# Performance work log

Hardware: AMD Instinct MI355X
Metric: run time of the kernel (lower is better)

## Reference

```python
import jax, jax.numpy as jnp
import numpy as np

B, TGT, SRC, DIM = 8, 1024, 1024, 1024

def setup_inputs() -> dict:
    key = jax.random.key(0)
    k1, k2, k3, k4, k5 = jax.random.split(key, 5)
    s = 1.0 / np.sqrt(DIM)
    return {
        "input": jax.random.normal(k1, (B, TGT, DIM), dtype=jnp.float32),
        "context": jax.random.normal(k2, (B, SRC, DIM), dtype=jnp.float32),
        "context_lengths": jax.random.randint(k3, (B,), 1, SRC + 1, dtype=jnp.int64 if jax.config.jax_enable_x64 else jnp.int32),
        "W_in": jax.random.normal(k4, (DIM, DIM), dtype=jnp.float32) * s,   # torch Linear weight [out,in]
        "W_out": jax.random.normal(k5, (DIM, 2 * DIM), dtype=jnp.float32) * s,
    }

def reference(input, context, context_lengths, W_in, W_out):
    # GlobalAttention, attn_type='general', include_rnn=True, dropout=0 (identity)
    # score: (W_in @ h_t) . h_s  -> [B, TGT, SRC]
    h_t = jnp.einsum('btd,ed->bte', input, W_in)
    align = jnp.einsum('bte,bse->bts', h_t, context)
    # mask positions >= length with -inf before softmax over source dim
    mask = jnp.arange(align.shape[-1])[None, :] < context_lengths[:, None]  # [B, SRC]
    align = jnp.where(mask[:, None, :], align, -jnp.inf)
    align_vectors = jax.nn.softmax(align, axis=-1)                         # [B, TGT, SRC]
    c = jnp.einsum('bts,bsd->btd', align_vectors, context)                 # context vector
    concat = jnp.concatenate([c, input], axis=-1)                          # [B, TGT, 2*DIM]
    attn_h = jnp.tanh(jnp.einsum('btf,df->btd', concat, W_out))            # linear_out (no bias) + tanh
    return attn_h, align_vectors
```

## Files before the change

### kernel.cpp

```cpp
#include <hip/hip_runtime.h>

typedef __attribute__((ext_vector_type(8))) short short8;
typedef __attribute__((ext_vector_type(4))) float f32x4;

#define DIM  1024
#define BT   8192
#define NBAT 8

__device__ __forceinline__ unsigned short f2bf(float x){
  union { float f; unsigned u; } un; un.f = x;
  unsigned r = un.u + 0x7fffu + ((un.u >> 16) & 1u);
  return (unsigned short)(r >> 16);
}
__device__ __forceinline__ float bf2f(unsigned short h){
  union { unsigned u; float f; } un; un.u = ((unsigned)h) << 16;
  return un.f;
}

__global__ void split_kernel(const float* __restrict__ x,
                             unsigned short* __restrict__ hi,
                             unsigned short* __restrict__ lo,
                             int n4){
  int stride = gridDim.x * blockDim.x;
  for (int i = blockIdx.x * blockDim.x + threadIdx.x; i < n4; i += stride){
    float4 v = ((const float4*)x)[i];
    ushort4 h, l;
    h.x = f2bf(v.x); l.x = f2bf(v.x - bf2f(h.x));
    h.y = f2bf(v.y); l.y = f2bf(v.y - bf2f(h.y));
    h.z = f2bf(v.z); l.z = f2bf(v.z - bf2f(h.z));
    h.w = f2bf(v.w); l.w = f2bf(v.w - bf2f(h.w));
    ((ushort4*)hi)[i] = h;
    ((ushort4*)lo)[i] = l;
  }
}

__global__ void cvt_kernel(const float* __restrict__ x,
                           unsigned short* __restrict__ hi, int n4){
  int stride = gridDim.x * blockDim.x;
  for (int i = blockIdx.x * blockDim.x + threadIdx.x; i < n4; i += stride){
    float4 v = ((const float4*)x)[i];
    ushort4 h;
    h.x = f2bf(v.x); h.y = f2bf(v.y); h.z = f2bf(v.z); h.w = f2bf(v.w);
    ((ushort4*)hi)[i] = h;
  }
}

__global__ void ctx_prep_kernel(const float* __restrict__ ctx,
                                unsigned short* __restrict__ hi,
                                unsigned short* __restrict__ lo,
                                unsigned short* __restrict__ ctxT){
  __shared__ unsigned short t[64][65];
  int bz = blockIdx.z;
  int s0 = blockIdx.x << 6, d0 = blockIdx.y << 6;
  int tx = threadIdx.x, ty = threadIdx.y;
  const size_t base = (((size_t)bz << 10) + s0) * DIM + d0;
  const float* src = ctx + base;
  unsigned short* hrow = hi + base;
  unsigned short* lrow = lo + base;
  #pragma unroll
  for (int i = ty; i < 64; i += 4){
    float v = src[(size_t)i * DIM + tx];
    unsigned short h = f2bf(v);
    hrow[(size_t)i * DIM + tx] = h;
    lrow[(size_t)i * DIM + tx] = f2bf(v - bf2f(h));
    t[i][tx] = h;
  }
  __syncthreads();
  unsigned short* dst = ctxT + (((size_t)bz << 10) + d0) * DIM + s0;
  #pragma unroll
  for (int i = ty; i < 64; i += 4)
    dst[(size_t)i * DIM + tx] = t[tx][i];
}

__global__ __launch_bounds__(256) void softmax_kernel(float* __restrict__ sc,
                                                      unsigned short* __restrict__ Pb,
                                                      const int* __restrict__ lens){
  const int row = blockIdx.x;
  const int len = lens[row >> 10];
  const int tid = threadIdx.x;
  const int lane = tid & 63, wid = tid >> 6;
  float* rp = sc + ((size_t)row << 10);
  const int s0 = tid << 2;
  float4 v;
  if (s0 < len) v = ((const float4*)rp)[tid];
  else          v = (float4){0.f, 0.f, 0.f, 0.f};
  float x0 = (s0 + 0 < len) ? v.x : -INFINITY;
  float x1 = (s0 + 1 < len) ? v.y : -INFINITY;
  float x2 = (s0 + 2 < len) ? v.z : -INFINITY;
  float x3 = (s0 + 3 < len) ? v.w : -INFINITY;
  float wmax = fmaxf(fmaxf(x0, x1), fmaxf(x2, x3));
  #pragma unroll
  for (int o = 32; o > 0; o >>= 1) wmax = fmaxf(wmax, __shfl_xor(wmax, o));
  __shared__ float red[8];
  if (lane == 0) red[wid] = wmax;
  __syncthreads();
  float mx = fmaxf(fmaxf(red[0], red[1]), fmaxf(red[2], red[3]));
  float e0 = (s0 + 0 < len) ? __expf(x0 - mx) : 0.f;
  float e1 = (s0 + 1 < len) ? __expf(x1 - mx) : 0.f;
  float e2 = (s0 + 2 < len) ? __expf(x2 - mx) : 0.f;
  float e3 = (s0 + 3 < len) ? __expf(x3 - mx) : 0.f;
  float ws = e0 + e1 + e2 + e3;
  #pragma unroll
  for (int o = 32; o > 0; o >>= 1) ws += __shfl_xor(ws, o);
  if (lane == 0) red[4 + wid] = ws;
  __syncthreads();
  float inv = 1.f / (red[4] + red[5] + red[6] + red[7]);
  float4 p; p.x = e0 * inv; p.y = e1 * inv; p.z = e2 * inv; p.w = e3 * inv;
  ((float4*)rp)[tid] = p;
  ushort4 pb; pb.x = f2bf(p.x); pb.y = f2bf(p.y); pb.z = f2bf(p.z); pb.w = f2bf(p.w);
  ((ushort4*)(Pb + ((size_t)row << 10)))[tid] = pb;
}

__device__ __forceinline__ int lds_off(int r, int kb){
  return r * 64 + (((kb ^ ((r >> 1) & 3))) << 4);
}

__device__ __forceinline__ void gld16(void* lds, const void* g){
  __builtin_amdgcn_global_load_lds(
      (__attribute__((address_space(1))) void*)(g),
      (__attribute__((address_space(3))) void*)(lds), 16, 0, 0);
}

#define TILEA 16384
#define TILEB 8192

template<int EPI, int NT, int KSPLIT, int SM>
__global__ __launch_bounds__(512, 2) void gemm_pipe_kernel(
    const unsigned short* __restrict__ Ah,  const unsigned short* __restrict__ Al,
    const unsigned short* __restrict__ Ah2, const unsigned short* __restrict__ Al2,
    const unsigned short* __restrict__ Bh,  const unsigned short* __restrict__ Bl,
    int lda, int ldb,
    float* __restrict__ outF, unsigned short* __restrict__ o1,
    unsigned short* __restrict__ o2, int ldo)
{
  constexpr int OFF_AL = TILEA;
  constexpr int OFF_BH = (SM == 0) ? 2 * TILEA : TILEA;
  constexpr int OFF_BL = OFF_BH + TILEB;
  constexpr int BUFSZ_T = (SM == 2) ? (OFF_BH + TILEB) : (OFF_BL + TILEB);

  __shared__ __align__(16) char sm0[BUFSZ_T];
  __shared__ __align__(16) char sm1[BUFSZ_T];
  __shared__ __align__(16) char sm2[BUFSZ_T];

  const int tid  = threadIdx.x;
  const int lane = tid & 63;
  const int w    = tid >> 6;

  int bx = blockIdx.x, by = blockIdx.y;
  {
    int o = bx + (by << 3);
    int xcd = o & 7, j = o >> 3;
    bx = j & 7;
    by = xcd * (gridDim.y >> 3) + (j >> 3);
  }
  const int m0 = by << 8;
  const int n0 = bx << 7;

  const unsigned short* gAh  = Ah  + (size_t)m0 * lda;
  const unsigned short* gAl  = Al  + (size_t)m0 * lda;
  const unsigned short* gAh2 = Ah2 + (size_t)m0 * lda;
  const unsigned short* gAl2 = Al2 + (size_t)m0 * lda;
  const unsigned short* gBh  = Bh  + (size_t)n0 * ldb;
  const unsigned short* gBl  = Bl  + (size_t)n0 * ldb;

  const int rA0 = (w << 5) + (lane >> 2);
  const int rA1 = rA0 + 16;
  const int rB0 = (w << 4) + (lane >> 2);
  const int cA0 = ((lane & 3) ^ ((rA0 >> 1) & 3)) << 3;
  const int cA1 = ((lane & 3) ^ ((rA1 >> 1) & 3)) << 3;
  const int cB0 = ((lane & 3) ^ ((rB0 >> 1) & 3)) << 3;
  const unsigned short* pAh0  = gAh  + (size_t)rA0 * lda + cA0;
  const unsigned short* pAh1  = gAh  + (size_t)rA1 * lda + cA1;
  const unsigned short* pAl0  = gAl  + (size_t)rA0 * lda + cA0;
  const unsigned short* pAl1  = gAl  + (size_t)rA1 * lda + cA1;
  const unsigned short* pAh20 = gAh2 + (size_t)rA0 * lda + cA0;
  const unsigned short* pAh21 = gAh2 + (size_t)rA1 * lda + cA1;
  const unsigned short* pAl20 = gAl2 + (size_t)rA0 * lda + cA0;
  const unsigned short* pAl21 = gAl2 + (size_t)rA1 * lda + cA1;
  const unsigned short* pBh0  = gBh  + (size_t)rB0 * ldb + cB0;
  const unsigned short* pBl0  = gBl  + (size_t)rB0 * ldb + cB0;
  const int dA0 = (w << 5) << 6;
  const int dA1 = dA0 + (16 << 6);
  const int dB0 = (w << 4) << 6;

  f32x4 acc[4][4];
  #pragma unroll
  for (int m = 0; m < 4; m++)
    #pragma unroll
    for (int n = 0; n < 4; n++)
      acc[m][n] = (f32x4){0.f, 0.f, 0.f, 0.f};

  const int wr = (w >> 1) << 6;
  const int wc = (w & 1) << 6;
  const int fr = lane & 15;
  const int kb = lane >> 4;

  short8 ah, al, bh[4], bl[4];

#define STAGE(WR, KS) do { int _k = (KS);                                   \
    const unsigned short *_s0, *_s1;                                        \
    if (KSPLIT < NT * 32 && _k >= KSPLIT){                                  \
      int _q = _k - KSPLIT;                                                 \
      _s0 = pAh20 + _q; _s1 = pAh21 + _q;                                   \
    } else { _s0 = pAh0 + _k; _s1 = pAh1 + _k; }                            \
    gld16(WR + dA0, _s0);                                                   \
    gld16(WR + dA1, _s1);                                                   \
    if constexpr (SM == 0){                                                 \
      const unsigned short *_s2, *_s3;                                      \
      if (KSPLIT < NT * 32 && _k >= KSPLIT){                                \
        int _q = _k - KSPLIT;                                               \
        _s2 = pAl20 + _q; _s3 = pAl21 + _q;                                 \
      } else { _s2 = pAl0 + _k; _s3 = pAl1 + _k; }                          \
      gld16(WR + OFF_AL + dA0, _s2);                                        \
      gld16(WR + OFF_AL + dA1, _s3);                                        \
    }                                                                       \
    gld16(WR + OFF_BH + dB0, pBh0 + _k);                                    \
    if constexpr (SM != 2)                                                  \
      gld16(WR + OFF_BL + dB0, pBl0 + _k);                                  \
  } while(0)

#define READS_B(RD) do {                                                    \
    _Pragma("unroll")                                                       \
    for (int n = 0; n < 4; n++){                                            \
      int off = lds_off(wc + n * 16 + fr, kb);                              \
      bh[n] = *(const short8*)((RD) + OFF_BH + off);                        \
      if constexpr (SM != 2)                                                \
        bl[n] = *(const short8*)((RD) + OFF_BL + off);                      \
    }                                                                       \
  } while(0)

#define READS_A(RD, M) do {                                                 \
    int off = lds_off(wr + (M) * 16 + fr, kb);                              \
    ah = *(const short8*)((RD) + off);                                      \
    if constexpr (SM == 0) al = *(const short8*)((RD) + OFF_AL + off);      \
  } while(0)

#define MFMA_M(M) do {                                                      \
    __builtin_amdgcn_s_setprio(1);                                          \
    _Pragma("unroll")                                                       \
    for (int n = 0; n < 4; n++){                                            \
      acc[M][n] = __builtin_amdgcn_mfma_f32_16x16x32_bf16(ah, bh[n], acc[M][n], 0, 0, 0); \
      if constexpr (SM != 2)                                                \
        acc[M][n] = __builtin_amdgcn_mfma_f32_16x16x32_bf16(ah, bl[n], acc[M][n], 0, 0, 0); \
      if constexpr (SM == 0)                                                \
        acc[M][n] = __builtin_amdgcn_mfma_f32_16x16x32_bf16(al, bh[n], acc[M][n], 0, 0, 0); \
    }                                                                       \
    __builtin_amdgcn_s_setprio(0);                                          \
  } while(0)

#define BAR() do { __builtin_amdgcn_s_barrier();                            \
                   asm volatile("" ::: "memory"); } while(0)
#define LGKM0() asm volatile("s_waitcnt lgkmcnt(0)" ::: "memory")
#define VMCNT_STEP() do {                                                   \
    if constexpr (SM == 0)      asm volatile("s_waitcnt vmcnt(6)" ::: "memory"); \
    else if constexpr (SM == 1) asm volatile("s_waitcnt vmcnt(4)" ::: "memory"); \
    else                        asm volatile("s_waitcnt vmcnt(3)" ::: "memory"); \
  } while(0)

#define STEP(RD, WR, T) do {                                                \
    int _ks = (((T) + 2 < NT) ? (T) + 2 : NT - 1) << 5;   \
    READS_B(RD); READS_A(RD, 0);                                            \
    STAGE(WR, _ks);                                                         \
    BAR(); LGKM0(); MFMA_M(0); BAR();                                       \
    READS_A(RD, 1);                                                        \
    BAR(); LGKM0(); MFMA_M(1); BAR();                                       \
    READS_A(RD, 2);                                                        \
    BAR(); LGKM0(); MFMA_M(2); BAR();                                       \
    READS_A(RD, 3);                                                        \
    BAR(); LGKM0(); MFMA_M(3);                                              \
    VMCNT_STEP();                                                           \
    BAR();                                                                  \
  } while(0)

  STAGE(sm0, 0);
  STAGE(sm1, 32);
  VMCNT_STEP();
  BAR();

  for (int t = 0; t < NT; t += 3){
    STEP(sm0, sm2, t);
    if (t + 1 < NT) STEP(sm1, sm0, t + 1);
    if (t + 2 < NT) STEP(sm2, sm1, t + 2);
  }
#undef STAGE
#undef READS_B
#undef READS_A
#undef MFMA_M
#undef BAR
#undef LGKM0
#undef VMCNT_STEP
#undef STEP

  const int rbase = (lane >> 4) << 2;
  const int cbase = lane & 15;
  #pragma unroll
  for (int m = 0; m < 4; m++){
    #pragma unroll
    for (int n = 0; n < 4; n++){
      f32x4 v = acc[m][n];
      int col = n0 + wc + n * 16 + cbase;
      #pragma unroll
      for (int j = 0; j < 4; j++){
        int row = m0 + wr + m * 16 + rbase + j;
        float val = v[j];
        size_t idx = (size_t)row * ldo + col;
        if (EPI == 0){
          unsigned short h = f2bf(val);
          o1[idx] = h;
          o2[idx] = f2bf(val - bf2f(h));
        } else {
          outF[idx] = tanhf(val);
        }
      }
    }
  }
}

template<bool SPLIT, int EPI>
__global__ __launch_bounds__(256, 2) void gemm_kernel(
    const unsigned short* __restrict__ Ah, const unsigned short* __restrict__ Al,
    const unsigned short* __restrict__ Bh, const unsigned short* __restrict__ Bl,
    int K, int lda, int ldb,
    long long aStride, long long bStride, long long oStride,
    float* __restrict__ outF, unsigned short* __restrict__ o1,
    unsigned short* __restrict__ o2, int ldo,
    const int* __restrict__ lens, int lmode)
{
  constexpr int TILE = 128 * 64;
  __shared__ __align__(16) char smem[(SPLIT ? 4 : 2) * TILE];
  char* sAh = smem;
  char* sBh = smem + TILE;
  char* sAl = smem + (SPLIT ? 2 : 0) * TILE;
  char* sBl = smem + (SPLIT ? 3 : 0) * TILE;

  const int tid  = threadIdx.x;
  const int lane = tid & 63;
  const int wid  = tid >> 6;
  const int z    = blockIdx.z;

  int bx = blockIdx.x, by = blockIdx.y;
  if (gridDim.x == 8 && gridDim.y == 8){
    int o = bx + (by << 3);
    int k = o & 7, j = o >> 3;
    bx = ((k & 3) << 1) | (j & 1);  by = ((k >> 2) << 2) | (j >> 1);
  }
  const int m0 = by * 128;
  const int n0 = bx * 128;

  int Keff = K;
  if (lmode){
    const int len = lens[z];
    if (lmode == 1 && n0 >= len) return;
    if (lmode == 2){
      int kc = (len + 31) & ~31;
      Keff = kc < K ? kc : K;
    }
  }

  const unsigned short* gAh = Ah + (size_t)z * aStride + (size_t)m0 * lda;
  const unsigned short* gBh = Bh + (size_t)z * bStride + (size_t)n0 * ldb;
  const unsigned short* gAl = SPLIT ? (Al + (size_t)z * aStride + (size_t)m0 * lda) : (const unsigned short*)0;
  const unsigned short* gBl = SPLIT ? (Bl + (size_t)z * bStride + (size_t)n0 * ldb) : (const unsigned short*)0;

  const int rS0 = (wid << 5) + (lane >> 2);
  const int rS1 = rS0 + 16;
  const int cS0 = ((lane & 3) ^ ((rS0 >> 1) & 3)) << 3;
  const int cS1 = ((lane & 3) ^ ((rS1 >> 1) & 3)) << 3;
  const int dS0 = (wid << 5) << 6;
  const int dS1 = dS0 + (16 << 6);
  const unsigned short* qAh0 = gAh + (size_t)rS0 * lda + cS0;
  const unsigned short* qAh1 = gAh + (size_t)rS1 * lda + cS1;
  const unsigned short* qBh0 = gBh + (size_t)rS0 * ldb + cS0;
  const unsigned short* qBh1 = gBh + (size_t)rS1 * ldb + cS1;
  const unsigned short* qAl0 = SPLIT ? (gAl + (size_t)rS0 * lda + cS0) : (const unsigned short*)0;
  const unsigned short* qAl1 = SPLIT ? (gAl + (size_t)rS1 * lda + cS1) : (const unsigned short*)0;
  const unsigned short* qBl0 = SPLIT ? (gBl + (size_t)rS0 * ldb + cS0) : (const unsigned short*)0;
  const unsigned short* qBl1 = SPLIT ? (gBl + (size_t)rS1 * ldb + cS1) : (const unsigned short*)0;

  f32x4 acc[4][4];
  #pragma unroll
  for (int m = 0; m < 4; m++)
    #pragma unroll
    for (int n = 0; n < 4; n++)
      acc[m][n] = (f32x4){0.f, 0.f, 0.f, 0.f};

  const int wr = (wid >> 1) * 64;
  const int wc = (wid & 1) * 64;
  const int fr = lane & 15;
  const int kb = lane >> 4;

  for (int k0 = 0; k0 < Keff; k0 += 32){
    __syncthreads();
    gld16(sAh + dS0, qAh0 + k0);
    gld16(sAh + dS1, qAh1 + k0);
    gld16(sBh + dS0, qBh0 + k0);
    gld16(sBh + dS1, qBh1 + k0);
    if (SPLIT){
      gld16(sAl + dS0, qAl0 + k0);
      gld16(sAl + dS1, qAl1 + k0);
      gld16(sBl + dS0, qBl0 + k0);
      gld16(sBl + dS1, qBl1 + k0);
    }
    __syncthreads();

    short8 ah[4], bh[4], al[4], bl[4];
    #pragma unroll
    for (int m = 0; m < 4; m++){
      int off = lds_off(wr + m * 16 + fr, kb);
      ah[m] = *(const short8*)(sAh + off);
      if (SPLIT) al[m] = *(const short8*)(sAl + off);
    }
    #pragma unroll
    for (int n = 0; n < 4; n++){
      int off = lds_off(wc + n * 16 + fr, kb);
      bh[n] = *(const short8*)(sBh + off);
      if (SPLIT) bl[n] = *(const short8*)(sBl + off);
    }
    #pragma unroll
    for (int m = 0; m < 4; m++)
      #pragma unroll
      for (int n = 0; n < 4; n++){
        acc[m][n] = __builtin_amdgcn_mfma_f32_16x16x32_bf16(ah[m], bh[n], acc[m][n], 0, 0, 0);
        if (SPLIT){
          acc[m][n] = __builtin_amdgcn_mfma_f32_16x16x32_bf16(ah[m], bl[n], acc[m][n], 0, 0, 0);
          acc[m][n] = __builtin_amdgcn_mfma_f32_16x16x32_bf16(al[m], bh[n], acc[m][n], 0, 0, 0);
        }
      }
  }

  const int rbase = (lane >> 4) * 2 * 2;
  const int cbase = lane & 15;
  #pragma unroll
  for (int m = 0; m < 4; m++){
    #pragma unroll
    for (int n = 0; n < 4; n++){
      f32x4 v = acc[m][n];
      int col = n0 + wc + n * 16 + cbase;
      #pragma unroll
      for (int j = 0; j < 4; j++){
        int row = m0 + wr + m * 16 + rbase + j;
        float val = v[j];
        size_t idx = (size_t)row * ldo + col;
        if (EPI == 0){
          unsigned short h = f2bf(val);
          o1[(size_t)z * oStride + idx] = h;
          o2[(size_t)z * oStride + idx] = f2bf(val - bf2f(h));
        } else if (EPI == 1){
          outF[(size_t)z * oStride + idx] = val;
        } else if (EPI == 4){
          o1[(size_t)z * oStride + idx] = f2bf(val);
        } else {
          outF[idx] = tanhf(val);
        }
      }
    }
  }
}

extern "C" void kernel_launch(void* const* d_in, const int* in_sizes, int n_in,
                              void* d_out, int out_size, void* d_ws, size_t ws_size,
                              hipStream_t stream){
  const float* input   = (const float*)d_in[0];
  const float* context = (const float*)d_in[1];
  const int*   lens    = (const int*)d_in[2];
  const float* Win     = (const float*)d_in[3];
  const float* Wout    = (const float*)d_in[4];
  float* attn  = (float*)d_out;
  float* align = attn + (size_t)BT * DIM;

  char* ws = (char*)d_ws;
  size_t off = 0;
  auto alloc = [&](size_t bytes) -> char* {
    char* p = ws + off; off += (bytes + 255) & ~(size_t)255; return p;
  };
  const size_t MTD = (size_t)BT * DIM;
  unsigned short* in_hi = (unsigned short*)alloc(MTD * 2);
  unsigned short* in_lo = (unsigned short*)alloc(MTD * 2);
  unsigned short* cx_hi = (unsigned short*)alloc(MTD * 2);
  unsigned short* cx_lo = (unsigned short*)alloc(MTD * 2);
  unsigned short* wi_hi = (unsigned short*)alloc((size_t)DIM * DIM * 2);
  unsigned short* wi_lo = (unsigned short*)alloc((size_t)DIM * DIM * 2);
  unsigned short* ht_hi = (unsigned short*)alloc(MTD * 2);
  unsigned short* ht_lo = (unsigned short*)alloc(MTD * 2);
  unsigned short* cxT   = (unsigned short*)alloc(MTD * 2);
  unsigned short* c_hi  = (unsigned short*)alloc(MTD * 2);
  unsigned short* wo_hi = (unsigned short*)alloc((size_t)DIM * 2 * DIM * 2);
  unsigned short* p_bf  = cx_hi;
  if (off > ws_size) return;

  split_kernel<<<4096, 256, 0, stream>>>(input, in_hi, in_lo, (int)(MTD >> 2));
  split_kernel<<<1024, 256, 0, stream>>>(Win, wi_hi, wi_lo, (DIM * DIM) >> 2);
  cvt_kernel<<<2048, 256, 0, stream>>>(Wout, wo_hi, (DIM * 2 * DIM) >> 2);
  ctx_prep_kernel<<<dim3(16, 16, NBAT), dim3(64, 4), 0, stream>>>(context, cx_hi, cx_lo, cxT);

  gemm_pipe_kernel<0, 32, 1024, 0><<<dim3(8, 32), 512, 0, stream>>>(
      in_hi, in_lo, in_hi, in_lo, wi_hi, wi_lo, DIM, DIM,
      nullptr, ht_hi, ht_lo, DIM);
  gemm_kernel<true, 1><<<dim3(8, 8, NBAT), 256, 0, stream>>>(
      ht_hi, ht_lo, cx_hi, cx_lo, DIM, DIM, DIM,
      (long long)DIM * 1024, (long long)DIM * 1024, (long long)DIM * 1024,
      align, nullptr, nullptr, DIM, lens, 1);
  softmax_kernel<<<BT, 256, 0, stream>>>(align, p_bf, lens);
  gemm_kernel<false, 4><<<dim3(8, 8, NBAT), 256, 0, stream>>>(
      p_bf, nullptr, cxT, nullptr, DIM, DIM, DIM,
      (long long)DIM * 1024, (long long)DIM * 1024, (long long)1024 * 1024,
      nullptr, c_hi, nullptr, DIM, lens, 2);
  gemm_pipe_kernel<3, 64, 1024, 2><<<dim3(8, 32), 512, 0, stream>>>(
      c_hi, c_hi, in_hi, in_hi, wo_hi, wo_hi, DIM, 2 * DIM,
      attn, nullptr, nullptr, DIM);
}
```

Before: 228.5 us.

## Use 128x128-tile triple-buffered bf16 GEMM for output projection

Replaces the output-projection GEMM (concat[c,input] times W_out, with a tanh epilogue) with a new kernel. It uses 128x128 tiles, 256 threads and two blocks per CU, launched on a 512-block grid instead of 256 larger blocks. The kernel triple-buffers LDS tiles with async global loads, remaps blocks across XCDs, and splits MFMA work per M-subtile with barriers and setprio. The aim is better occupancy, more blocks in flight and more overlap of loads with compute. In exchange there are more barriers per K step and smaller per-block reuse of the B operand.

```diff
diff --git a/kernel.cpp b/kernel.cpp
--- a/kernel.cpp
+++ b/kernel.cpp
@@ -311,6 +311,152 @@
         } else {
           outF[idx] = tanhf(val);
         }
+      }
+    }
+  }
+}
+
+template<int EPI, int NT, int KSPLIT>
+__global__ __launch_bounds__(256, 2) void gemm_pipe128_kernel(
+    const unsigned short* __restrict__ Ah, const unsigned short* __restrict__ Ah2,
+    const unsigned short* __restrict__ Bh,
+    int lda, int ldb,
+    float* __restrict__ outF, unsigned short* __restrict__ o1, int ldo)
+{
+  constexpr int TA  = 8192;
+  constexpr int OFF_B = TA;
+  constexpr int BUF = 2 * TA;
+
+  __shared__ __align__(16) char sm0[BUF];
+  __shared__ __align__(16) char sm1[BUF];
+  __shared__ __align__(16) char sm2[BUF];
+
+  const int tid  = threadIdx.x;
+  const int lane = tid & 63;
+  const int w    = tid >> 6;
+
+  int bx = blockIdx.x, by = blockIdx.y;
+  {
+    int o = bx + (by << 3);
+    int xcd = o & 7, j = o >> 3;
+    bx = j & 7;
+    by = xcd * (gridDim.y >> 3) + (j >> 3);
+  }
+  const int m0 = by << 7;
+  const int n0 = bx << 7;
+
+  const unsigned short* gAh  = Ah  + (size_t)m0 * lda;
+  const unsigned short* gAh2 = Ah2 + (size_t)m0 * lda;
+  const unsigned short* gBh  = Bh  + (size_t)n0 * ldb;
+
+  const int rS0 = (w << 5) + (lane >> 2);
+  const int rS1 = rS0 + 16;
+  const int cS0 = ((lane & 3) ^ ((rS0 >> 1) & 3)) << 3;
+  const int cS1 = ((lane & 3) ^ ((rS1 >> 1) & 3)) << 3;
+  const unsigned short* pA0  = gAh  + (size_t)rS0 * lda + cS0;
+  const unsigned short* pA1  = gAh  + (size_t)rS1 * lda + cS1;
+  const unsigned short* pA20 = gAh2 + (size_t)rS0 * lda + cS0;
+  const unsigned short* pA21 = gAh2 + (size_t)rS1 * lda + cS1;
+  const unsigned short* pB0  = gBh  + (size_t)rS0 * ldb + cS0;
+  const unsigned short* pB1  = gBh  + (size_t)rS1 * ldb + cS1;
+  const int dS0 = (w << 5) << 6;
+  const int dS1 = dS0 + (16 << 6);
+
+  f32x4 acc[4][4];
+  #pragma unroll
+  for (int m = 0; m < 4; m++)
+    #pragma unroll
+    for (int n = 0; n < 4; n++)
+      acc[m][n] = (f32x4){0.f, 0.f, 0.f, 0.f};
+
+  const int wr = (w >> 1) << 6;
+  const int wc = (w & 1) << 6;
+  const int fr = lane & 15;
+  const int kb = lane >> 4;
+
+  short8 ah, bh[4];
+
+#define STAGE(WR, KS) do { int _k = (KS);                                   \
+    const unsigned short *_s0, *_s1;                                        \
+    if (_k >= KSPLIT){ int _q = _k - KSPLIT; _s0 = pA20 + _q; _s1 = pA21 + _q; } \
+    else             { _s0 = pA0 + _k;       _s1 = pA1 + _k; }              \
+    gld16(WR + dS0, _s0);                                                   \
+    gld16(WR + dS1, _s1);                                                   \
+    gld16(WR + OFF_B + dS0, pB0 + _k);                                      \
+    gld16(WR + OFF_B + dS1, pB1 + _k);                                      \
+  } while(0)
+
+#define READS_B(RD) do {                                                    \
+    _Pragma("unroll")                                                       \
+    for (int n = 0; n < 4; n++)                                             \
+      bh[n] = *(const short8*)((RD) + OFF_B + lds_off(wc + n * 16 + fr, kb)); \
+  } while(0)
+
+#define READS_A(RD, M)                                                      \
+    ah = *(const short8*)((RD) + lds_off(wr + (M) * 16 + fr, kb))
+
+#define MFMA_M(M) do {                                                      \
+    __builtin_amdgcn_s_setprio(1);                                          \
+    _Pragma("unroll")                                                       \
+    for (int n = 0; n < 4; n++)                                             \
+      acc[M][n] = __builtin_amdgcn_mfma_f32_16x16x32_bf16(ah, bh[n], acc[M][n], 0, 0, 0); \
+    __builtin_amdgcn_s_setprio(0);                                          \
+  } while(0)
+
+#define BAR() do { __builtin_amdgcn_s_barrier();                            \
+                   asm volatile("" ::: "memory"); } while(0)
+#define LGKM0() asm volatile("s_waitcnt lgkmcnt(0)" ::: "memory")
+#define VMCNT4() asm volatile("s_waitcnt vmcnt(4)" ::: "memory")
+
+#define STEP(RD, WR, T) do {                                                \
+    int _ks = (((T) + 2 < NT) ? (T) + 2 : NT - 1) << 5;   \
+    READS_B(RD); READS_A(RD, 0);                                            \
+    STAGE(WR, _ks);                                                         \
+    BAR(); LGKM0(); MFMA_M(0); BAR();                                       \
+    READS_A(RD, 1);                                                        \
+    BAR(); LGKM0(); MFMA_M(1); BAR();                                       \
+    READS_A(RD, 2);                                                        \
+    BAR(); LGKM0(); MFMA_M(2); BAR();                                       \
+    READS_A(RD, 3);                                                        \
+    BAR(); LGKM0(); MFMA_M(3);                                              \
+    VMCNT4();                                                               \
+    BAR();                                                                  \
+  } while(0)
+
+  STAGE(sm0, 0);
+  STAGE(sm1, 32);
+  VMCNT4();
+  BAR();
+
+  for (int t = 0; t < NT; t += 3){
+    STEP(sm0, sm2, t);
+    if (t + 1 < NT) STEP(sm1, sm0, t + 1);
+    if (t + 2 < NT) STEP(sm2, sm1, t + 2);
+  }
+#undef STAGE
+#undef READS_B
+#undef READS_A
+#undef MFMA_M
+#undef BAR
+#undef LGKM0
+#undef VMCNT4
+#undef STEP
+
+  const int rbase = (lane >> 4) << 2;
+  const int cbase = lane & 15;
+  #pragma unroll
+  for (int m = 0; m < 4; m++){
+    #pragma unroll
+    for (int n = 0; n < 4; n++){
+      f32x4 v = acc[m][n];
+      int col = n0 + wc + n * 16 + cbase;
+      #pragma unroll
+      for (int j = 0; j < 4; j++){
+        int row = m0 + wr + m * 16 + rbase + j;
+        float val = v[j];
+        size_t idx = (size_t)row * ldo + col;
+        if (EPI == 3) outF[idx] = tanhf(val);
+        else          o1[idx] = f2bf(val);
       }
     }
   }
@@ -505,7 +651,7 @@
       p_bf, nullptr, cxT, nullptr, DIM, DIM, DIM,
       (long long)DIM * 1024, (long long)DIM * 1024, (long long)1024 * 1024,
       nullptr, c_hi, nullptr, DIM, lens, 2);
-  gemm_pipe_kernel<3, 64, 1024, 2><<<dim3(8, 32), 512, 0, stream>>>(
-      c_hi, c_hi, in_hi, in_hi, wo_hi, wo_hi, DIM, 2 * DIM,
-      attn, nullptr, nullptr, DIM);
-}
+  gemm_pipe128_kernel<3, 64, 1024><<<dim3(8, 64), 256, 0, stream>>>(
+      c_hi, in_hi, wo_hi, DIM, 2 * DIM,
+      attn, nullptr, DIM);
+}
```

New measurement: 222.8 us. -2.5%, faster.
